# Optimization experiments

Measured on AMD Instinct MI355X. Metric: run time of the kernel, lower is better.

## Reference

```python
import jax, jax.numpy as jnp
import numpy as np

H = 28
W = 28
CIN = 128
COUT = 32
K = 3
SHIFT = 1  # fixed shift_direction (original draws +/-1 at init)


def setup_inputs() -> dict:
    key = jax.random.key(0)
    kx, kw = jax.random.split(key)
    x = jax.random.normal(kx, (512, CIN, H, W), dtype=jnp.float32)
    w = jax.random.normal(kw, (COUT, CIN, K), dtype=jnp.float32)
    return {"x": x, "w": w}


def reference(x, w):
    # Original: reshape to (B, C*H, W, 1), unfold with kernel (3,1) pad (1,0)
    # -> conv with kernel 3 along the W axis, then einsum contracts channel
    # and kernel dims (128->32), then roll by +1 along H.
    B = x.shape[0]
    xp = jnp.pad(x, ((0, 0), (0, 0), (0, 0), (1, 1)))  # pad W by 1 each side
    # windows: (B, CIN, H, K, W) — mirrors the unfold+reshape to (1,128,28,3,28)
    win = jnp.stack([xp[..., k:k + W] for k in range(K)], axis=3)
    # einsum 'limkn, jik -> ljmn' with batch dim: contract channel i and tap k
    y = jnp.einsum('bihkn,jik->bjhn', win, w)  # (B, COUT, H, W)
    # permute->(B,H,COUT,W), roll along H, permute back == roll on axis 2 here
    y = jnp.roll(y, SHIFT, axis=2)
    return y
```

## Files before the change

kernel.cpp:

```cpp
#include <hip/hip_runtime.h>
#include <hip/hip_bf16.h>

#define CIN_  128
#define H_    28
#define W_    28
#define COUT_ 32
#define B_    512

typedef __attribute__((ext_vector_type(8))) short short8;
typedef __attribute__((ext_vector_type(4))) float f32x4;

__device__ __forceinline__ short f2bf(float f) {
    __hip_bfloat16 h = __float2bfloat16(f);
    union { __hip_bfloat16 h; short s; } u; u.h = h;
    return u.s;
}

__global__ void prep_w_kernel(const float* __restrict__ w, short* __restrict__ wsA) {
    int t = blockIdx.x * 256 + threadIdx.x;
    int frag = t >> 9;
    int rem  = t & 511;
    int l = rem >> 3;
    int j = rem & 7;
    int mt = frag / 12;
    int kc = frag % 12;
    int tap = kc >> 2;
    int i  = (kc & 3) * 32 + (l >> 4) * 8 + j;
    int jo = mt * 16 + (l & 15);
    wsA[t] = f2bf(w[(jo * CIN_ + i) * 3 + tap]);
}

template<bool USE_WS>
__global__ __launch_bounds__(256, 5)
void conv_kernel(const float* __restrict__ x, const float* __restrict__ w,
                 const short* __restrict__ wsA, float* __restrict__ out) {
    __shared__ short lds[4][30 * CIN_];
    const int tid = threadIdx.x;
    const int wv  = tid >> 6;
    const int l   = tid & 63;
    const int hg  = blockIdx.x;
    const int b   = blockIdx.y;
    const int h0  = hg * 4;

    const float* xb = x + (size_t)b * (CIN_ * H_ * W_);

    {
        int s   = (tid & 63) * 4;
        int row = (s >= 128) ? 29 : 0;
        int c   = s & 127;
        *reinterpret_cast<ulong1*>(&lds[wv][row * CIN_ + c]) = ulong1{0};
    }

#pragma unroll
    for (int half = 0; half < 2; ++half) {
        f32x4 vb[7];
#pragma unroll
        for (int it = 0; it < 7; ++it) {
            int f4 = (half * 7 + it) * 256 + tid;
            int i  = f4 / 28;
            int q  = f4 % 28;
            vb[it] = *reinterpret_cast<const f32x4*>(xb + i * (H_ * W_) + h0 * W_ + q * 4);
        }
#pragma unroll
        for (int it = 0; it < 7; ++it) {
            int f4 = (half * 7 + it) * 256 + tid;
            int i  = f4 / 28;
            int q  = f4 % 28;
            int hl = q / 7;
            int w4 = q % 7;
            short* buf = lds[hl];
#pragma unroll
            for (int e = 0; e < 4; ++e) {
                int wt   = w4 * 4 + e + 1;
                int sidx = wt * CIN_ + ((((i >> 3) ^ (wt & 15)) << 3) | (i & 7));
                buf[sidx] = f2bf(vb[it][e]);
            }
        }
    }
    __syncthreads();

    short* wbuf = lds[wv];
    const int h = h0 + wv;

    f32x4 acc[2][2];
#pragma unroll
    for (int mt = 0; mt < 2; ++mt)
#pragma unroll
        for (int nt = 0; nt < 2; ++nt)
#pragma unroll
            for (int q = 0; q < 4; ++q) acc[mt][nt][q] = 0.0f;

#pragma unroll
    for (int half = 0; half < 2; ++half) {
        short8 a0[6], a1[6];
        if (USE_WS) {
#pragma unroll
            for (int k6 = 0; k6 < 6; ++k6) {
                int kc = half * 6 + k6;
                a0[k6] = *reinterpret_cast<const short8*>(wsA + kc * 512 + l * 8);
                a1[k6] = *reinterpret_cast<const short8*>(wsA + (12 + kc) * 512 + l * 8);
            }
        } else {
#pragma unroll
            for (int k6 = 0; k6 < 6; ++k6) {
                int kc  = half * 6 + k6;
                int tap = kc >> 2;
                int ib  = (kc & 3) * 32 + (l >> 4) * 8;
#pragma unroll
                for (int j = 0; j < 8; ++j) {
                    a0[k6][j] = f2bf(w[((l & 15) * CIN_ + ib + j) * 3 + tap]);
                    a1[k6][j] = f2bf(w[((16 + (l & 15)) * CIN_ + ib + j) * 3 + tap]);
                }
            }
        }
#pragma unroll
        for (int k6 = 0; k6 < 6; ++k6) {
            int kc  = half * 6 + k6;
            int tap = kc >> 2;
            int c   = (kc & 3) * 4 + (l >> 4);
#pragma unroll
            for (int nt = 0; nt < 2; ++nt) {
                int wt  = nt * 16 + (l & 15) + tap;
                int wtc = wt > 29 ? 29 : wt;
                const short8 bfrag = *reinterpret_cast<const short8*>(
                    &wbuf[wtc * CIN_ + ((c ^ (wtc & 15)) << 3)]);
                acc[0][nt] = __builtin_amdgcn_mfma_f32_16x16x32_bf16(
                    a0[k6], bfrag, acc[0][nt], 0, 0, 0);
                acc[1][nt] = __builtin_amdgcn_mfma_f32_16x16x32_bf16(
                    a1[k6], bfrag, acc[1][nt], 0, 0, 0);
            }
        }
    }

    float* ob = out + (size_t)b * (COUT_ * H_ * W_);
    const int ho = (h + 1 == H_) ? 0 : (h + 1);
#pragma unroll
    for (int mt = 0; mt < 2; ++mt)
#pragma unroll
        for (int nt = 0; nt < 2; ++nt)
#pragma unroll
            for (int rr = 0; rr < 4; ++rr) {
                int j    = mt * 16 + (l >> 4) * 4 + rr;
                int wcol = nt * 16 + (l & 15);
                if (wcol < W_)
                    ob[(j * H_ + ho) * W_ + wcol] = acc[mt][nt][rr];
            }
}

extern "C" void kernel_launch(void* const* d_in, const int* in_sizes, int n_in,
                              void* d_out, int out_size, void* d_ws, size_t ws_size,
                              hipStream_t stream) {
    (void)in_sizes; (void)n_in; (void)out_size;
    const float* x = (const float*)d_in[0];
    const float* w = (const float*)d_in[1];
    float* out = (float*)d_out;

    if (ws_size >= (size_t)(24 * 512 * sizeof(short))) {
        short* wsA = (short*)d_ws;
        prep_w_kernel<<<dim3(48), dim3(256), 0, stream>>>(w, wsA);
        conv_kernel<true><<<dim3(7, 512), dim3(256), 0, stream>>>(x, w, wsA, out);
    } else {
        conv_kernel<false><<<dim3(7, 512), dim3(256), 0, stream>>>(x, w, (const short*)nullptr, out);
    }
}
```

Baseline: 58.69 us.

## Stage output through LDS for vectorized stores, remap blocks across XCDs, batch loads

The output tile is staged through LDS so each thread writes 16-byte vectors along W, replacing scattered scalar stores. The grid is flattened and block IDs are remapped so consecutive logical tiles land on the same XCD, which should improve L2 locality. All 14 input vector loads are now issued before any conversion, raising memory-level parallelism at the cost of more registers. Two extra barriers are added for the LDS staging.

```diff
diff --git a/kernel.cpp b/kernel.cpp
--- a/kernel.cpp
+++ b/kernel.cpp
@@ -38,8 +38,11 @@
     const int tid = threadIdx.x;
     const int wv  = tid >> 6;
     const int l   = tid & 63;
-    const int hg  = blockIdx.x;
-    const int b   = blockIdx.y;
+
+    const int Bid = blockIdx.x;
+    const int L   = (Bid & 7) * 448 + (Bid >> 3);
+    const int b   = L / 7;
+    const int hg  = L % 7;
     const int h0  = hg * 4;
 
     const float* xb = x + (size_t)b * (CIN_ * H_ * W_);
@@ -51,36 +54,32 @@
         *reinterpret_cast<ulong1*>(&lds[wv][row * CIN_ + c]) = ulong1{0};
     }
 
+    f32x4 vb[14];
 #pragma unroll
-    for (int half = 0; half < 2; ++half) {
-        f32x4 vb[7];
+    for (int it = 0; it < 14; ++it) {
+        int f4 = it * 256 + tid;
+        int i  = f4 / 28;
+        int q  = f4 % 28;
+        vb[it] = *reinterpret_cast<const f32x4*>(xb + i * (H_ * W_) + h0 * W_ + q * 4);
+    }
 #pragma unroll
-        for (int it = 0; it < 7; ++it) {
-            int f4 = (half * 7 + it) * 256 + tid;
-            int i  = f4 / 28;
-            int q  = f4 % 28;
-            vb[it] = *reinterpret_cast<const f32x4*>(xb + i * (H_ * W_) + h0 * W_ + q * 4);
-        }
+    for (int it = 0; it < 14; ++it) {
+        int f4 = it * 256 + tid;
+        int i  = f4 / 28;
+        int q  = f4 % 28;
+        int hl = q / 7;
+        int w4 = q % 7;
+        short* buf = lds[hl];
 #pragma unroll
-        for (int it = 0; it < 7; ++it) {
-            int f4 = (half * 7 + it) * 256 + tid;
-            int i  = f4 / 28;
-            int q  = f4 % 28;
-            int hl = q / 7;
-            int w4 = q % 7;
-            short* buf = lds[hl];
-#pragma unroll
-            for (int e = 0; e < 4; ++e) {
-                int wt   = w4 * 4 + e + 1;
-                int sidx = wt * CIN_ + ((((i >> 3) ^ (wt & 15)) << 3) | (i & 7));
-                buf[sidx] = f2bf(vb[it][e]);
-            }
+        for (int e = 0; e < 4; ++e) {
+            int wt   = w4 * 4 + e + 1;
+            int sidx = wt * CIN_ + ((((i >> 3) ^ (wt & 15)) << 3) | (i & 7));
+            buf[sidx] = f2bf(vb[it][e]);
         }
     }
     __syncthreads();
 
     short* wbuf = lds[wv];
-    const int h = h0 + wv;
 
     f32x4 acc[2][2];
 #pragma unroll
@@ -131,9 +130,9 @@
             }
         }
     }
+    __syncthreads();
 
-    float* ob = out + (size_t)b * (COUT_ * H_ * W_);
-    const int ho = (h + 1 == H_) ? 0 : (h + 1);
+    float* arr = reinterpret_cast<float*>(&lds[0][0]);
 #pragma unroll
     for (int mt = 0; mt < 2; ++mt)
 #pragma unroll
@@ -143,8 +142,25 @@
                 int j    = mt * 16 + (l >> 4) * 4 + rr;
                 int wcol = nt * 16 + (l & 15);
                 if (wcol < W_)
-                    ob[(j * H_ + ho) * W_ + wcol] = acc[mt][nt][rr];
+                    arr[(j * 4 + wv) * W_ + wcol] = acc[mt][nt][rr];
             }
+    __syncthreads();
+
+    float* ob = out + (size_t)b * (COUT_ * H_ * W_);
+#pragma unroll
+    for (int it = 0; it < 4; ++it) {
+        int c = it * 256 + tid;
+        if (c < 896) {
+            int j  = c / 28;
+            int q  = c % 28;
+            int hl = q / 7;
+            int w4 = q % 7;
+            int ho = h0 + hl + 1;
+            if (ho >= H_) ho -= H_;
+            f32x4 v = *reinterpret_cast<const f32x4*>(&arr[(j * 4 + hl) * W_ + w4 * 4]);
+            *reinterpret_cast<f32x4*>(ob + (j * H_ + ho) * W_ + w4 * 4) = v;
+        }
+    }
 }
 
 extern "C" void kernel_launch(void* const* d_in, const int* in_sizes, int n_in,
@@ -158,8 +174,8 @@
     if (ws_size >= (size_t)(24 * 512 * sizeof(short))) {
         short* wsA = (short*)d_ws;
         prep_w_kernel<<<dim3(48), dim3(256), 0, stream>>>(w, wsA);
-        conv_kernel<true><<<dim3(7, 512), dim3(256), 0, stream>>>(x, w, wsA, out);
+        conv_kernel<true><<<dim3(3584), dim3(256), 0, stream>>>(x, w, wsA, out);
     } else {
-        conv_kernel<false><<<dim3(7, 512), dim3(256), 0, stream>>>(x, w, (const short*)nullptr, out);
+        conv_kernel<false><<<dim3(3584), dim3(256), 0, stream>>>(x, w, (const short*)nullptr, out);
     }
 }
```

Result: no change. 59.84 us (+2.0%).

## Process two tiles per block with register prefetch of the next tile

Applied to the files above, without the earlier changes.

Each block now handles two consecutive (batch, row-group) tiles instead of one, halving the grid to 1792 blocks. The second tile's global loads are issued into registers while the first tile is converted into LDS and computed, so load latency overlaps with MFMA work. A workgroup-to-tile remap spreads consecutive block IDs across the tile space, and the A-fragment loads are split per M-tile to cut register pressure. Occupancy is lowered to 4 waves per SIMD to make room for the 14-vector prefetch buffer, and an extra barrier is added between tiles.

```diff
diff --git a/kernel.cpp b/kernel.cpp
--- a/kernel.cpp
+++ b/kernel.cpp
@@ -31,18 +31,29 @@
 }
 
 template<bool USE_WS>
-__global__ __launch_bounds__(256, 5)
+__global__ __launch_bounds__(256, 4)
 void conv_kernel(const float* __restrict__ x, const float* __restrict__ w,
                  const short* __restrict__ wsA, float* __restrict__ out) {
     __shared__ short lds[4][30 * CIN_];
     const int tid = threadIdx.x;
     const int wv  = tid >> 6;
     const int l   = tid & 63;
-    const int hg  = blockIdx.x;
-    const int b   = blockIdx.y;
-    const int h0  = hg * 4;
 
-    const float* xb = x + (size_t)b * (CIN_ * H_ * W_);
+    const int k  = blockIdx.x;
+    const int T0 = ((k & 7) * 224 + (k >> 3)) * 2;
+
+    f32x4 vb[14];
+    {
+        const int bb = T0 / 7, hh = T0 % 7;
+        const float* xb = x + (size_t)bb * (CIN_ * H_ * W_) + hh * (4 * W_);
+#pragma unroll
+        for (int it = 0; it < 14; ++it) {
+            int f4 = it * 256 + tid;
+            int i  = f4 / 28;
+            int q  = f4 % 28;
+            vb[it] = *reinterpret_cast<const f32x4*>(xb + i * (H_ * W_) + q * 4);
+        }
+    }
 
     {
         int s   = (tid & 63) * 4;
@@ -52,18 +63,14 @@
     }
 
 #pragma unroll
-    for (int half = 0; half < 2; ++half) {
-        f32x4 vb[7];
+    for (int t = 0; t < 2; ++t) {
+        const int T  = T0 + t;
+        const int bt = T / 7;
+        const int h0 = (T % 7) * 4;
+
 #pragma unroll
-        for (int it = 0; it < 7; ++it) {
-            int f4 = (half * 7 + it) * 256 + tid;
-            int i  = f4 / 28;
-            int q  = f4 % 28;
-            vb[it] = *reinterpret_cast<const f32x4*>(xb + i * (H_ * W_) + h0 * W_ + q * 4);
-        }
-#pragma unroll
-        for (int it = 0; it < 7; ++it) {
-            int f4 = (half * 7 + it) * 256 + tid;
+        for (int it = 0; it < 14; ++it) {
+            int f4 = it * 256 + tid;
             int i  = f4 / 28;
             int q  = f4 % 28;
             int hl = q / 7;
@@ -76,75 +83,97 @@
                 buf[sidx] = f2bf(vb[it][e]);
             }
         }
-    }
-    __syncthreads();
 
-    short* wbuf = lds[wv];
-    const int h = h0 + wv;
+        if (t == 0) {
+            const int Tn = T0 + 1;
+            const int bb = Tn / 7, hh = Tn % 7;
+            const float* xb = x + (size_t)bb * (CIN_ * H_ * W_) + hh * (4 * W_);
+#pragma unroll
+            for (int it = 0; it < 14; ++it) {
+                int f4 = it * 256 + tid;
+                int i  = f4 / 28;
+                int q  = f4 % 28;
+                vb[it] = *reinterpret_cast<const f32x4*>(xb + i * (H_ * W_) + q * 4);
+            }
+            __builtin_amdgcn_sched_barrier(0);
+        }
 
-    f32x4 acc[2][2];
+        asm volatile("s_waitcnt lgkmcnt(0)" ::: "memory");
+        __builtin_amdgcn_sched_barrier(0);
+        __builtin_amdgcn_s_barrier();
+        __builtin_amdgcn_sched_barrier(0);
+
+        f32x4 acc[2][2];
 #pragma unroll
-    for (int mt = 0; mt < 2; ++mt)
+        for (int mt = 0; mt < 2; ++mt)
 #pragma unroll
-        for (int nt = 0; nt < 2; ++nt)
+            for (int nt = 0; nt < 2; ++nt)
 #pragma unroll
-            for (int q = 0; q < 4; ++q) acc[mt][nt][q] = 0.0f;
+                for (int q = 0; q < 4; ++q) acc[mt][nt][q] = 0.0f;
 
+        short* wbuf = lds[wv];
 #pragma unroll
-    for (int half = 0; half < 2; ++half) {
-        short8 a0[6], a1[6];
-        if (USE_WS) {
+        for (int half = 0; half < 2; ++half) {
 #pragma unroll
-            for (int k6 = 0; k6 < 6; ++k6) {
-                int kc = half * 6 + k6;
-                a0[k6] = *reinterpret_cast<const short8*>(wsA + kc * 512 + l * 8);
-                a1[k6] = *reinterpret_cast<const short8*>(wsA + (12 + kc) * 512 + l * 8);
-            }
-        } else {
+            for (int mt = 0; mt < 2; ++mt) {
+                short8 a6[6];
+                if (USE_WS) {
 #pragma unroll
-            for (int k6 = 0; k6 < 6; ++k6) {
-                int kc  = half * 6 + k6;
-                int tap = kc >> 2;
-                int ib  = (kc & 3) * 32 + (l >> 4) * 8;
+                    for (int k6 = 0; k6 < 6; ++k6)
+                        a6[k6] = *reinterpret_cast<const short8*>(
+                            wsA + (mt * 12 + half * 6 + k6) * 512 + l * 8);
+                } else {
 #pragma unroll
-                for (int j = 0; j < 8; ++j) {
-                    a0[k6][j] = f2bf(w[((l & 15) * CIN_ + ib + j) * 3 + tap]);
-                    a1[k6][j] = f2bf(w[((16 + (l & 15)) * CIN_ + ib + j) * 3 + tap]);
+                    for (int k6 = 0; k6 < 6; ++k6) {
+                        int kc  = half * 6 + k6;
+                        int tap = kc >> 2;
+                        int ib  = (kc & 3) * 32 + (l >> 4) * 8;
+#pragma unroll
+                        for (int j = 0; j < 8; ++j)
+                            a6[k6][j] = f2bf(w[((mt * 16 + (l & 15)) * CIN_ + ib + j) * 3 + tap]);
+                    }
+                }
+#pragma unroll
+                for (int k6 = 0; k6 < 6; ++k6) {
+                    int kc  = half * 6 + k6;
+                    int tap = kc >> 2;
+                    int c   = (kc & 3) * 4 + (l >> 4);
+#pragma unroll
+                    for (int nt = 0; nt < 2; ++nt) {
+                        int wt  = nt * 16 + (l & 15) + tap;
+                        int wtc = wt > 29 ? 29 : wt;
+                        const short8 bfrag = *reinterpret_cast<const short8*>(
+                            &wbuf[wtc * CIN_ + ((c ^ (wtc & 15)) << 3)]);
+                        acc[mt][nt] = __builtin_amdgcn_mfma_f32_16x16x32_bf16(
+                            a6[k6], bfrag, acc[mt][nt], 0, 0, 0);
+                    }
                 }
             }
         }
+
+        {
+            float* ob = out + (size_t)bt * (COUT_ * H_ * W_);
+            const int h  = h0 + wv;
+            const int ho = (h + 1 == H_) ? 0 : (h + 1);
 #pragma unroll
-        for (int k6 = 0; k6 < 6; ++k6) {
-            int kc  = half * 6 + k6;
-            int tap = kc >> 2;
-            int c   = (kc & 3) * 4 + (l >> 4);
+            for (int mt = 0; mt < 2; ++mt)
 #pragma unroll
-            for (int nt = 0; nt < 2; ++nt) {
-                int wt  = nt * 16 + (l & 15) + tap;
-                int wtc = wt > 29 ? 29 : wt;
-                const short8 bfrag = *reinterpret_cast<const short8*>(
-                    &wbuf[wtc * CIN_ + ((c ^ (wtc & 15)) << 3)]);
-                acc[0][nt] = __builtin_amdgcn_mfma_f32_16x16x32_bf16(
-                    a0[k6], bfrag, acc[0][nt], 0, 0, 0);
-                acc[1][nt] = __builtin_amdgcn_mfma_f32_16x16x32_bf16(
-                    a1[k6], bfrag, acc[1][nt], 0, 0, 0);
-            }
+                for (int nt = 0; nt < 2; ++nt)
+#pragma unroll
+                    for (int rr = 0; rr < 4; ++rr) {
+                        int j    = mt * 16 + (l >> 4) * 4 + rr;
+                        int wcol = nt * 16 + (l & 15);
+                        if (wcol < W_)
+                            ob[(j * H_ + ho) * W_ + wcol] = acc[mt][nt][rr];
+                    }
+        }
+
+        if (t == 0) {
+            __builtin_amdgcn_sched_barrier(0);
+            __builtin_amdgcn_s_barrier();
+            __builtin_amdgcn_sched_barrier(0);
         }
     }
-
-    float* ob = out + (size_t)b * (COUT_ * H_ * W_);
-    const int ho = (h + 1 == H_) ? 0 : (h + 1);
-#pragma unroll
-    for (int mt = 0; mt < 2; ++mt)
-#pragma unroll
-        for (int nt = 0; nt < 2; ++nt)
-#pragma unroll
-            for (int rr = 0; rr < 4; ++rr) {
-                int j    = mt * 16 + (l >> 4) * 4 + rr;
-                int wcol = nt * 16 + (l & 15);
-                if (wcol < W_)
-                    ob[(j * H_ + ho) * W_ + wcol] = acc[mt][nt][rr];
-            }
 }
 
 extern "C" void kernel_launch(void* const* d_in, const int* in_sizes, int n_in,
@@ -158,8 +187,8 @@
     if (ws_size >= (size_t)(24 * 512 * sizeof(short))) {
         short* wsA = (short*)d_ws;
         prep_w_kernel<<<dim3(48), dim3(256), 0, stream>>>(w, wsA);
-        conv_kernel<true><<<dim3(7, 512), dim3(256), 0, stream>>>(x, w, wsA, out);
+        conv_kernel<true><<<dim3(1792), dim3(256), 0, stream>>>(x, w, wsA, out);
     } else {
-        conv_kernel<false><<<dim3(7, 512), dim3(256), 0, stream>>>(x, w, (const short*)nullptr, out);
+        conv_kernel<false><<<dim3(1792), dim3(256), 0, stream>>>(x, w, (const short*)nullptr, out);
     }
 }
```

Result: slower. 130.4 us (+122.1%).
